# Kernel tuning notes

Hardware: AMD Instinct MI355X
Metric: run time of the kernel (lower is better)

Reference implementation:

```python
import jax, jax.numpy as jnp
import numpy as np

INPUT_SIZE = 40960
HIDDEN_SIZE = 128
OUTPUT_SIZE = 1
BATCH = 4096


def setup_inputs() -> dict:
    key = jax.random.key(0)
    k1, k2, k3, kw1, kw2, kw3 = jax.random.split(key, 6)
    x1 = jax.random.uniform(k1, (BATCH, INPUT_SIZE), dtype=jnp.float32)
    x2 = jax.random.uniform(k2, (BATCH, INPUT_SIZE), dtype=jnp.float32)
    turn = jax.random.randint(k3, (BATCH,), 0, 2, dtype=jnp.int32)
    # nn.Linear weights: [out_features, in_features], kaiming-uniform-ish scale
    s1 = 1.0 / np.sqrt(INPUT_SIZE)
    s2 = 1.0 / np.sqrt(2 * HIDDEN_SIZE)
    w_us = jax.random.uniform(kw1, (HIDDEN_SIZE, INPUT_SIZE), minval=-s1, maxval=s1, dtype=jnp.float32)
    w_them = jax.random.uniform(kw2, (HIDDEN_SIZE, INPUT_SIZE), minval=-s1, maxval=s1, dtype=jnp.float32)
    w2 = jax.random.uniform(kw3, (OUTPUT_SIZE, 2 * HIDDEN_SIZE), minval=-s2, maxval=s2, dtype=jnp.float32)
    return {"x1": x1, "x2": x2, "turn": turn, "w_us": w_us, "w_them": w_them, "w2": w2}


def reference(x1, x2, turn, w_us, w_them, w2):
    # acc1 = relu(fc1_us(x1)); acc2 = relu(fc1_them(x2))
    acc1 = jax.nn.relu(jnp.einsum('bi,hi->bh', x1, w_us))   # [B, H]
    acc2 = jax.nn.relu(jnp.einsum('bi,hi->bh', x2, w_them)) # [B, H]
    x = jnp.concatenate((acc1, acc2), axis=1)               # [B, 2H]
    return jnp.einsum('bh,oh->bo', x, w2)                   # [B, 1]
```

## Files before the change

kernel.cpp:

```cpp
#include <hip/hip_runtime.h>

#define B_ROWS 4096
#define K_DIM  40960
#define H_DIM  128
#define BM     128
#define BK     64
#define KSPLIT 8
#define KCHUNK (K_DIM / KSPLIT)
#define NT     (KCHUNK / BK)
#define MT     (B_ROWS / BM)

typedef __attribute__((ext_vector_type(4))) float f32x4;
typedef __attribute__((ext_vector_type(8))) short short8;

static_assert(KSPLIT * KCHUNK == K_DIM, "ksplit");
static_assert((NT & 1) == 0, "NT even");

__device__ float g_acc[2u * B_ROWS * H_DIM];

__device__ __forceinline__ unsigned pkbf(float a, float b) {
  unsigned ua = __float_as_uint(a), ub = __float_as_uint(b);
  ua = (ua + 0x7fffu + ((ua >> 16) & 1u)) >> 16;
  ub = (ub + 0x7fffu + ((ub >> 16) & 1u)) & 0xffff0000u;
  return ua | ub;
}

template <bool ATOMIC>
__global__ __launch_bounds__(512, 4) void nnue_stage1(
    const float* __restrict__ x1, const float* __restrict__ x2,
    const float* __restrict__ wus, const float* __restrict__ wthem,
    float* __restrict__ part) {
  __shared__ ushort ldsA[2][BM][BK];
  __shared__ ushort ldsB[2][H_DIM][BK];

  const int t = threadIdx.x;

  const int bid  = blockIdx.x;
  const int xcd  = bid & 7;
  const int slot = bid >> 3;
  const int g    = xcd + 8 * (slot >> 5);
  const int mt   = slot & 31;
  const int mat  = g & 1;
  const int ks   = g >> 1;

  const float* __restrict__ X = mat ? x2 : x1;
  const float* __restrict__ W = mat ? wthem : wus;
  const size_t kb0 = (size_t)ks * KCHUNK;

  const int r0 = t >> 4;
  const int c0 = (t & 15) * 4;

  const float* gA = X + (size_t)(mt * BM + r0) * K_DIM + kb0 + c0;
  const float* gB = W + (size_t)r0 * K_DIM + kb0 + c0;

  const int wb0 =
      r0 * 128 + ((((t & 15) >> 1) ^ (r0 & 7)) << 4) + ((t & 1) * 8);

  const int l   = t & 63;
  const int w   = t >> 6;
  const int wr  = w >> 2;
  const int wc  = w & 3;
  const int fr  = l & 15;
  const int lhi = l >> 4;

  int offA[4], offB[2];
  #pragma unroll
  for (int i = 0; i < 4; ++i) {
    const int ra = wr * 64 + i * 16 + fr;
    offA[i] = ra * 128 + ((lhi ^ (ra & 7)) << 4);
  }
  #pragma unroll
  for (int j = 0; j < 2; ++j) {
    const int cb = wc * 32 + j * 16 + fr;
    offB[j] = cb * 128 + ((lhi ^ (cb & 7)) << 4);
  }

  f32x4 acc[4][2] = {};
  f32x4 sA0[4], sA1[4], sB[4];

#define LBAR()                                                              \
  do {                                                                      \
    asm volatile("s_waitcnt lgkmcnt(0)" ::: "memory");                      \
    __builtin_amdgcn_s_barrier();                                           \
    __builtin_amdgcn_sched_barrier(0);                                      \
  } while (0)

#define ISSUE_A(S_, kt_)                                                    \
  do {                                                                      \
    const float* pa = gA + (size_t)(kt_)*BK;                                \
    _Pragma("unroll") for (int r = 0; r < 4; ++r)                           \
        S_[r] = __builtin_nontemporal_load(                                 \
            (const f32x4*)(pa + (size_t)r * 32 * K_DIM));                   \
  } while (0)

#define ISSUE_B(kt_)                                                        \
  do {                                                                      \
    const float* pb = gB + (size_t)(kt_)*BK;                                \
    _Pragma("unroll") for (int r = 0; r < 4; ++r)                           \
        sB[r] = *(const f32x4*)(pb + (size_t)r * 32 * K_DIM);               \
  } while (0)

#define STAGE_A(S_, buf_)                                                   \
  do {                                                                      \
    char* bA = (char*)ldsA + (buf_)*16384 + wb0;                            \
    _Pragma("unroll") for (int r = 0; r < 4; ++r) {                         \
      uint2 u;                                                              \
      u.x = pkbf(S_[r][0], S_[r][1]);                                       \
      u.y = pkbf(S_[r][2], S_[r][3]);                                       \
      *(uint2*)(bA + r * 4096) = u;                                         \
    }                                                                       \
  } while (0)

#define STAGE_B(buf_)                                                       \
  do {                                                                      \
    char* bB = (char*)ldsB + (buf_)*16384 + wb0;                            \
    _Pragma("unroll") for (int r = 0; r < 4; ++r) {                         \
      uint2 u;                                                              \
      u.x = pkbf(sB[r][0], sB[r][1]);                                       \
      u.y = pkbf(sB[r][2], sB[r][3]);                                       \
      *(uint2*)(bB + r * 4096) = u;                                         \
    }                                                                       \
  } while (0)

#define COMPUTE(buf_)                                                       \
  do {                                                                      \
    const char* bA = (const char*)ldsA + (buf_)*16384;                      \
    const char* bB = (const char*)ldsB + (buf_)*16384;                      \
    _Pragma("unroll") for (int kb = 0; kb < 2; ++kb) {                      \
      const int kx = kb * 64;                                               \
      short8 af[4], bg[2];                                                  \
      _Pragma("unroll") for (int i = 0; i < 4; ++i)                         \
          af[i] = *(const short8*)(bA + (offA[i] ^ kx));                    \
      _Pragma("unroll") for (int j = 0; j < 2; ++j)                         \
          bg[j] = *(const short8*)(bB + (offB[j] ^ kx));                    \
      _Pragma("unroll") for (int i = 0; i < 4; ++i)                         \
          _Pragma("unroll") for (int j = 0; j < 2; ++j)                     \
              acc[i][j] = __builtin_amdgcn_mfma_f32_16x16x32_bf16(          \
                  af[i], bg[j], acc[i][j], 0, 0, 0);                        \
    }                                                                       \
  } while (0)

  ISSUE_A(sA0, 0);
  ISSUE_A(sA1, 1);
  ISSUE_B(0);

  for (int kt = 0; kt < NT; kt += 2) {
    STAGE_A(sA0, 0);
    STAGE_B(0);
    LBAR();
    ISSUE_B(kt + 1);
    if (kt + 2 < NT) ISSUE_A(sA0, kt + 2);
    COMPUTE(0);
    STAGE_A(sA1, 1);
    STAGE_B(1);
    LBAR();
    if (kt + 2 < NT) {
      ISSUE_B(kt + 2);
      if (kt + 3 < NT) ISSUE_A(sA1, kt + 3);
    }
    COMPUTE(1);
  }

#undef LBAR
#undef ISSUE_A
#undef ISSUE_B
#undef STAGE_A
#undef STAGE_B
#undef COMPUTE

  if (!ATOMIC) {
    float* dst = part + (((size_t)mat * KSPLIT + ks) * B_ROWS) * (size_t)H_DIM;
    #pragma unroll
    for (int i = 0; i < 4; ++i)
      #pragma unroll
      for (int j = 0; j < 2; ++j)
        #pragma unroll
        for (int r = 0; r < 4; ++r) {
          const int rowg = mt * BM + wr * 64 + i * 16 + (lhi << 2) + r;
          const int colg = wc * 32 + j * 16 + fr;
          __builtin_nontemporal_store(acc[i][j][r],
                                      &dst[(size_t)rowg * H_DIM + colg]);
        }
  } else {
    float* dst = g_acc + (size_t)mat * B_ROWS * H_DIM;
    #pragma unroll
    for (int i = 0; i < 4; ++i)
      #pragma unroll
      for (int j = 0; j < 2; ++j)
        #pragma unroll
        for (int r = 0; r < 4; ++r) {
          const int rowg = mt * BM + wr * 64 + i * 16 + (lhi << 2) + r;
          const int colg = wc * 32 + j * 16 + fr;
          atomicAdd(&dst[(size_t)rowg * H_DIM + colg], acc[i][j][r]);
        }
  }
}

__global__ void nnue_zero_acc() {
  const unsigned i = blockIdx.x * 256 + threadIdx.x;
  if (i < 2u * B_ROWS * H_DIM) g_acc[i] = 0.f;
}

template <int KS>
__global__ __launch_bounds__(512) void nnue_stage2(
    const float* __restrict__ part, const float* __restrict__ w2,
    float* __restrict__ out) {
  const float* p = part ? part : (const float*)g_acc;
  const int t = threadIdx.x;
  const int l = t & 63, w = t >> 6;
  const int b = blockIdx.x * 8 + w;
  float a0 = 0.f, a1 = 0.f, a2 = 0.f, a3 = 0.f;
  #pragma unroll
  for (int ks = 0; ks < KS; ++ks) {
    const float* p0 = p + ((size_t)ks * B_ROWS + b) * H_DIM;
    const float* p1 = p + (((size_t)KS + ks) * B_ROWS + b) * H_DIM;
    a0 += __builtin_nontemporal_load(&p0[l]);
    a1 += __builtin_nontemporal_load(&p0[l + 64]);
    a2 += __builtin_nontemporal_load(&p1[l]);
    a3 += __builtin_nontemporal_load(&p1[l + 64]);
  }
  float sv = fmaxf(a0, 0.f) * w2[l] + fmaxf(a1, 0.f) * w2[l + 64] +
             fmaxf(a2, 0.f) * w2[l + 128] + fmaxf(a3, 0.f) * w2[l + 192];
  #pragma unroll
  for (int off = 32; off; off >>= 1) sv += __shfl_xor(sv, off, 64);
  if (l == 0) out[b] = sv;
}

extern "C" void kernel_launch(void* const* d_in, const int* in_sizes, int n_in,
                              void* d_out, int out_size, void* d_ws,
                              size_t ws_size, hipStream_t stream) {
  const float* x1    = (const float*)d_in[0];
  const float* x2    = (const float*)d_in[1];
  const float* wus   = (const float*)d_in[3];
  const float* wthem = (const float*)d_in[4];
  const float* w2    = (const float*)d_in[5];
  float* out = (float*)d_out;

  const size_t PART_BYTES =
      2ull * KSPLIT * B_ROWS * H_DIM * sizeof(float);

  if (ws_size >= PART_BYTES) {
    float* part = (float*)d_ws;
    nnue_stage1<false><<<MT * KSPLIT * 2, 512, 0, stream>>>(x1, x2, wus, wthem,
                                                            part);
    nnue_stage2<KSPLIT><<<B_ROWS / 8, 512, 0, stream>>>(part, w2, out);
  } else {
    nnue_zero_acc<<<(2 * B_ROWS * H_DIM + 255) / 256, 256, 0, stream>>>();
    nnue_stage1<true><<<MT * KSPLIT * 2, 512, 0, stream>>>(x1, x2, wus, wthem,
                                                           nullptr);
    nnue_stage2<1><<<B_ROWS / 8, 512, 0, stream>>>(nullptr, w2, out);
  }
}
```

Baseline: 275.6 us.

## Double K tile to 128 with contiguous 128-byte per-thread row loads

Raises the K tile from 64 to 128, halving the number of barrier-separated iterations, and reorganizes global loads so each thread reads 32 contiguous floats of one row instead of four rows. LDS staging changes to 16-byte writes into two 64-wide halves with an XOR swizzle, bf16 packing now uses the HIP intrinsic, and the partial-sum store and stage-2 loads drop the nontemporal hint. LDS per block doubles and launch bounds fall to 2 blocks per SM, trading occupancy and more live registers for fewer syncs and wider memory accesses.

```diff
diff --git a/kernel.cpp b/kernel.cpp
--- a/kernel.cpp
+++ b/kernel.cpp
@@ -1,10 +1,11 @@
 #include <hip/hip_runtime.h>
+#include <hip/hip_bf16.h>
 
 #define B_ROWS 4096
 #define K_DIM  40960
 #define H_DIM  128
 #define BM     128
-#define BK     64
+#define BK     128
 #define KSPLIT 8
 #define KCHUNK (K_DIM / KSPLIT)
 #define NT     (KCHUNK / BK)
@@ -18,20 +19,19 @@
 
 __device__ float g_acc[2u * B_ROWS * H_DIM];
 
-__device__ __forceinline__ unsigned pkbf(float a, float b) {
-  unsigned ua = __float_as_uint(a), ub = __float_as_uint(b);
-  ua = (ua + 0x7fffu + ((ua >> 16) & 1u)) >> 16;
-  ub = (ub + 0x7fffu + ((ub >> 16) & 1u)) & 0xffff0000u;
-  return ua | ub;
+__device__ __forceinline__ unsigned pk2(float a, float b) {
+  union { __hip_bfloat162 h; unsigned u; } cv;
+  cv.h = __float22bfloat162_rn(make_float2(a, b));
+  return cv.u;
 }
 
 template <bool ATOMIC>
-__global__ __launch_bounds__(512, 4) void nnue_stage1(
+__global__ __launch_bounds__(512, 2) void nnue_stage1(
     const float* __restrict__ x1, const float* __restrict__ x2,
     const float* __restrict__ wus, const float* __restrict__ wthem,
     float* __restrict__ part) {
-  __shared__ ushort ldsA[2][BM][BK];
-  __shared__ ushort ldsB[2][H_DIM][BK];
+  __shared__ char ldsA[2 * 32768];
+  __shared__ char ldsB[2 * 32768];
 
   const int t = threadIdx.x;
 
@@ -47,14 +47,21 @@
   const float* __restrict__ W = mat ? wthem : wus;
   const size_t kb0 = (size_t)ks * KCHUNK;
 
-  const int r0 = t >> 4;
-  const int c0 = (t & 15) * 4;
-
-  const float* gA = X + (size_t)(mt * BM + r0) * K_DIM + kb0 + c0;
-  const float* gB = W + (size_t)r0 * K_DIM + kb0 + c0;
-
-  const int wb0 =
-      r0 * 128 + ((((t & 15) >> 1) ^ (r0 & 7)) << 4) + ((t & 1) * 8);
+  const int r0  = t >> 2;
+  const int seg = t & 3;
+
+  const float* gA = X + (size_t)(mt * BM + r0) * K_DIM + kb0 + seg * 32;
+  const float* gB = W + (size_t)r0 * K_DIM + kb0 + seg * 32;
+
+  int wb[4];
+  {
+    const int h   = seg >> 1;
+    const int cb0 = (seg & 1) * 4;
+    const int z   = r0 & 7;
+    #pragma unroll
+    for (int i = 0; i < 4; ++i)
+      wb[i] = h * 16384 + r0 * 128 + (((cb0 + i) ^ z) << 4);
+  }
 
   const int l   = t & 63;
   const int w   = t >> 6;
@@ -76,7 +83,7 @@
   }
 
   f32x4 acc[4][2] = {};
-  f32x4 sA0[4], sA1[4], sB[4];
+  f32x4 sA0[8], sA1[8], sB[8];
 
 #define LBAR()                                                              \
   do {                                                                      \
@@ -87,52 +94,43 @@
 
 #define ISSUE_A(S_, kt_)                                                    \
   do {                                                                      \
-    const float* pa = gA + (size_t)(kt_)*BK;                                \
-    _Pragma("unroll") for (int r = 0; r < 4; ++r)                           \
-        S_[r] = __builtin_nontemporal_load(                                 \
-            (const f32x4*)(pa + (size_t)r * 32 * K_DIM));                   \
+    const float* p = gA + (size_t)(kt_)*BK;                                 \
+    _Pragma("unroll") for (int r = 0; r < 8; ++r)                           \
+        S_[r] = __builtin_nontemporal_load((const f32x4*)(p + r * 4));      \
   } while (0)
 
 #define ISSUE_B(kt_)                                                        \
   do {                                                                      \
-    const float* pb = gB + (size_t)(kt_)*BK;                                \
-    _Pragma("unroll") for (int r = 0; r < 4; ++r)                           \
-        sB[r] = *(const f32x4*)(pb + (size_t)r * 32 * K_DIM);               \
-  } while (0)
-
-#define STAGE_A(S_, buf_)                                                   \
-  do {                                                                      \
-    char* bA = (char*)ldsA + (buf_)*16384 + wb0;                            \
-    _Pragma("unroll") for (int r = 0; r < 4; ++r) {                         \
-      uint2 u;                                                              \
-      u.x = pkbf(S_[r][0], S_[r][1]);                                       \
-      u.y = pkbf(S_[r][2], S_[r][3]);                                       \
-      *(uint2*)(bA + r * 4096) = u;                                         \
+    const float* p = gB + (size_t)(kt_)*BK;                                 \
+    _Pragma("unroll") for (int r = 0; r < 8; ++r)                           \
+        sB[r] = *(const f32x4*)(p + r * 4);                                 \
+  } while (0)
+
+#define STAGE(S_, ldsX_, buf_)                                              \
+  do {                                                                      \
+    char* b = (char*)ldsX_ + (buf_)*32768;                                  \
+    _Pragma("unroll") for (int i = 0; i < 4; ++i) {                         \
+      uint4 u;                                                              \
+      u.x = pk2(S_[2 * i][0], S_[2 * i][1]);                                \
+      u.y = pk2(S_[2 * i][2], S_[2 * i][3]);                                \
+      u.z = pk2(S_[2 * i + 1][0], S_[2 * i + 1][1]);                        \
+      u.w = pk2(S_[2 * i + 1][2], S_[2 * i + 1][3]);                        \
+      *(uint4*)(b + wb[i]) = u;                                             \
     }                                                                       \
   } while (0)
 
-#define STAGE_B(buf_)                                                       \
-  do {                                                                      \
-    char* bB = (char*)ldsB + (buf_)*16384 + wb0;                            \
-    _Pragma("unroll") for (int r = 0; r < 4; ++r) {                         \
-      uint2 u;                                                              \
-      u.x = pkbf(sB[r][0], sB[r][1]);                                       \
-      u.y = pkbf(sB[r][2], sB[r][3]);                                       \
-      *(uint2*)(bB + r * 4096) = u;                                         \
-    }                                                                       \
-  } while (0)
-
 #define COMPUTE(buf_)                                                       \
   do {                                                                      \
-    const char* bA = (const char*)ldsA + (buf_)*16384;                      \
-    const char* bB = (const char*)ldsB + (buf_)*16384;                      \
-    _Pragma("unroll") for (int kb = 0; kb < 2; ++kb) {                      \
-      const int kx = kb * 64;                                               \
+    const char* bA = (const char*)ldsA + (buf_)*32768;                      \
+    const char* bB = (const char*)ldsB + (buf_)*32768;                      \
+    _Pragma("unroll") for (int s = 0; s < 4; ++s) {                         \
+      const int ho = (s >> 1) * 16384;                                      \
+      const int ko = (s & 1) << 6;                                          \
       short8 af[4], bg[2];                                                  \
       _Pragma("unroll") for (int i = 0; i < 4; ++i)                         \
-          af[i] = *(const short8*)(bA + (offA[i] ^ kx));                    \
+          af[i] = *(const short8*)(bA + ho + (offA[i] ^ ko));               \
       _Pragma("unroll") for (int j = 0; j < 2; ++j)                         \
-          bg[j] = *(const short8*)(bB + (offB[j] ^ kx));                    \
+          bg[j] = *(const short8*)(bB + ho + (offB[j] ^ ko));               \
       _Pragma("unroll") for (int i = 0; i < 4; ++i)                         \
           _Pragma("unroll") for (int j = 0; j < 2; ++j)                     \
               acc[i][j] = __builtin_amdgcn_mfma_f32_16x16x32_bf16(          \
@@ -145,14 +143,14 @@
   ISSUE_B(0);
 
   for (int kt = 0; kt < NT; kt += 2) {
-    STAGE_A(sA0, 0);
-    STAGE_B(0);
+    STAGE(sA0, ldsA, 0);
+    STAGE(sB, ldsB, 0);
     LBAR();
     ISSUE_B(kt + 1);
     if (kt + 2 < NT) ISSUE_A(sA0, kt + 2);
     COMPUTE(0);
-    STAGE_A(sA1, 1);
-    STAGE_B(1);
+    STAGE(sA1, ldsA, 1);
+    STAGE(sB, ldsB, 1);
     LBAR();
     if (kt + 2 < NT) {
       ISSUE_B(kt + 2);
@@ -164,8 +162,7 @@
 #undef LBAR
 #undef ISSUE_A
 #undef ISSUE_B
-#undef STAGE_A
-#undef STAGE_B
+#undef STAGE
 #undef COMPUTE
 
   if (!ATOMIC) {
@@ -178,8 +175,7 @@
         for (int r = 0; r < 4; ++r) {
           const int rowg = mt * BM + wr * 64 + i * 16 + (lhi << 2) + r;
           const int colg = wc * 32 + j * 16 + fr;
-          __builtin_nontemporal_store(acc[i][j][r],
-                                      &dst[(size_t)rowg * H_DIM + colg]);
+          dst[(size_t)rowg * H_DIM + colg] = acc[i][j][r];
         }
   } else {
     float* dst = g_acc + (size_t)mat * B_ROWS * H_DIM;
@@ -214,10 +210,10 @@
   for (int ks = 0; ks < KS; ++ks) {
     const float* p0 = p + ((size_t)ks * B_ROWS + b) * H_DIM;
     const float* p1 = p + (((size_t)KS + ks) * B_ROWS + b) * H_DIM;
-    a0 += __builtin_nontemporal_load(&p0[l]);
-    a1 += __builtin_nontemporal_load(&p0[l + 64]);
-    a2 += __builtin_nontemporal_load(&p1[l]);
-    a3 += __builtin_nontemporal_load(&p1[l + 64]);
+    a0 += p0[l];
+    a1 += p0[l + 64];
+    a2 += p1[l];
+    a3 += p1[l + 64];
   }
   float sv = fmaxf(a0, 0.f) * w2[l] + fmaxf(a1, 0.f) * w2[l + 64] +
              fmaxf(a2, 0.f) * w2[l + 128] + fmaxf(a3, 0.f) * w2[l + 192];
```

Measured after the change: 828.2 us. 200% more time.

## Load A tiles as 128-float row spans covering two K-steps per issue

Applied to the files above, without the earlier changes.

Each thread now loads 8 consecutive rows × 4 floats spanning 128 columns of X, so one issue covers both K-tiles (two BK=64 buffers) with wider contiguous row segments. Half the threads stage into buffer 0 before the barrier, and the other half stage into buffer 1 after it. This replaces the separate sA0/sA1 double-issue. The aim is to improve global load coalescing and simplify the pipeline. Staging buffer 1 right after the barrier, while buffer 0 compute is running, looks safe because that buffer was last read in the previous iteration, but it shortens the prefetch distance for A.

```diff
diff --git a/kernel.cpp b/kernel.cpp
--- a/kernel.cpp
+++ b/kernel.cpp
@@ -47,13 +47,23 @@
   const float* __restrict__ W = mat ? wthem : wus;
   const size_t kb0 = (size_t)ks * KCHUNK;
 
+  const int ar = (t >> 5) * 8;
+  const int ac = (t & 31) * 4;
+  const float* gA = X + (size_t)(mt * BM + ar) * K_DIM + kb0 + ac;
+
+  int wbA[8];
+  {
+    const int c16 = (t & 15) >> 1;
+    const int p   = (t & 16) >> 4;
+    #pragma unroll
+    for (int j = 0; j < 8; ++j)
+      wbA[j] = p * 16384 + (ar + j) * 128 + ((c16 ^ j) << 4) + ((t & 1) * 8);
+  }
+
   const int r0 = t >> 4;
   const int c0 = (t & 15) * 4;
-
-  const float* gA = X + (size_t)(mt * BM + r0) * K_DIM + kb0 + c0;
   const float* gB = W + (size_t)r0 * K_DIM + kb0 + c0;
-
-  const int wb0 =
+  const int wbB0 =
       r0 * 128 + ((((t & 15) >> 1) ^ (r0 & 7)) << 4) + ((t & 1) * 8);
 
   const int l   = t & 63;
@@ -76,7 +86,7 @@
   }
 
   f32x4 acc[4][2] = {};
-  f32x4 sA0[4], sA1[4], sB[4];
+  f32x4 sA[8], sB[4];
 
 #define LBAR()                                                              \
   do {                                                                      \
@@ -85,35 +95,35 @@
     __builtin_amdgcn_sched_barrier(0);                                      \
   } while (0)
 
-#define ISSUE_A(S_, kt_)                                                    \
-  do {                                                                      \
-    const float* pa = gA + (size_t)(kt_)*BK;                                \
+#define ISSUE_A2(kt_)                                                       \
+  do {                                                                      \
+    const float* p = gA + (size_t)(kt_)*BK;                                 \
+    _Pragma("unroll") for (int j = 0; j < 8; ++j)                           \
+        sA[j] = __builtin_nontemporal_load(                                 \
+            (const f32x4*)(p + (size_t)j * K_DIM));                         \
+  } while (0)
+
+#define ISSUE_B(kt_)                                                        \
+  do {                                                                      \
+    const float* p = gB + (size_t)(kt_)*BK;                                 \
     _Pragma("unroll") for (int r = 0; r < 4; ++r)                           \
-        S_[r] = __builtin_nontemporal_load(                                 \
-            (const f32x4*)(pa + (size_t)r * 32 * K_DIM));                   \
-  } while (0)
-
-#define ISSUE_B(kt_)                                                        \
-  do {                                                                      \
-    const float* pb = gB + (size_t)(kt_)*BK;                                \
-    _Pragma("unroll") for (int r = 0; r < 4; ++r)                           \
-        sB[r] = *(const f32x4*)(pb + (size_t)r * 32 * K_DIM);               \
-  } while (0)
-
-#define STAGE_A(S_, buf_)                                                   \
-  do {                                                                      \
-    char* bA = (char*)ldsA + (buf_)*16384 + wb0;                            \
-    _Pragma("unroll") for (int r = 0; r < 4; ++r) {                         \
+        sB[r] = *(const f32x4*)(p + (size_t)r * 32 * K_DIM);                \
+  } while (0)
+
+#define STAGE_A_MINE()                                                      \
+  do {                                                                      \
+    char* bA = (char*)ldsA;                                                 \
+    _Pragma("unroll") for (int j = 0; j < 8; ++j) {                         \
       uint2 u;                                                              \
-      u.x = pkbf(S_[r][0], S_[r][1]);                                       \
-      u.y = pkbf(S_[r][2], S_[r][3]);                                       \
-      *(uint2*)(bA + r * 4096) = u;                                         \
+      u.x = pkbf(sA[j][0], sA[j][1]);                                       \
+      u.y = pkbf(sA[j][2], sA[j][3]);                                       \
+      *(uint2*)(bA + wbA[j]) = u;                                           \
     }                                                                       \
   } while (0)
 
 #define STAGE_B(buf_)                                                       \
   do {                                                                      \
-    char* bB = (char*)ldsB + (buf_)*16384 + wb0;                            \
+    char* bB = (char*)ldsB + (buf_)*16384 + wbB0;                           \
     _Pragma("unroll") for (int r = 0; r < 4; ++r) {                         \
       uint2 u;                                                              \
       u.x = pkbf(sB[r][0], sB[r][1]);                                       \
@@ -140,31 +150,27 @@
     }                                                                       \
   } while (0)
 
-  ISSUE_A(sA0, 0);
-  ISSUE_A(sA1, 1);
+  ISSUE_A2(0);
   ISSUE_B(0);
 
   for (int kt = 0; kt < NT; kt += 2) {
-    STAGE_A(sA0, 0);
+    if (!(t & 16)) STAGE_A_MINE();
     STAGE_B(0);
     LBAR();
+    if (t & 16) STAGE_A_MINE();
     ISSUE_B(kt + 1);
-    if (kt + 2 < NT) ISSUE_A(sA0, kt + 2);
+    if (kt + 2 < NT) ISSUE_A2(kt + 2);
     COMPUTE(0);
-    STAGE_A(sA1, 1);
     STAGE_B(1);
     LBAR();
-    if (kt + 2 < NT) {
-      ISSUE_B(kt + 2);
-      if (kt + 3 < NT) ISSUE_A(sA1, kt + 3);
-    }
+    if (kt + 2 < NT) ISSUE_B(kt + 2);
     COMPUTE(1);
   }
 
 #undef LBAR
-#undef ISSUE_A
+#undef ISSUE_A2
 #undef ISSUE_B
-#undef STAGE_A
+#undef STAGE_A_MINE
 #undef STAGE_B
 #undef COMPUTE
 
```

New measurement: 313.9 us. +13.9%, slower.
